# Kernel optimization log

Hardware: AMD Instinct MI355X
Metric: run time of the kernel (lower is better)

The kernel has to match this reference:

```python
import jax, jax.numpy as jnp
import numpy as np

EPS = jnp.float16(1e-8)

def setup_inputs() -> dict:
    key = jax.random.key(0)
    k1, k2, k3, k4 = jax.random.split(key, 4)
    B, S, D_IN, D_OUT = 4, 2048, 4096, 4096
    x = jax.random.normal(k1, (B, S, D_IN), dtype=jnp.float16)
    weight = jax.random.randint(k2, (D_OUT, D_IN), -127, 127, dtype=jnp.int32).astype(jnp.int8)
    weight_scales = (jax.random.uniform(k3, (D_OUT,), dtype=jnp.float32) * 0.02 + 0.001).astype(jnp.float16)
    bias = (jax.random.normal(k4, (1, D_OUT), dtype=jnp.float32) * 0.01).astype(jnp.float16)
    return {"x": x, "weight": weight, "weight_scales": weight_scales, "bias": bias}

def fake_quant_per_token(x):
    # per-token absmax fake quant to int8 range, stays fp16
    scales = jnp.max(jnp.abs(x), axis=-1, keepdims=True) / jnp.float16(127.0)
    scales = jnp.maximum(scales, EPS)
    return jnp.round(x / scales) * scales

def reference(x, weight, weight_scales, bias):
    # dequantize int8 weight with per-output-channel scales -> fp16 [out, in]
    w_fp16 = weight.astype(jnp.float16) * weight_scales[:, None]
    xq = fake_quant_per_token(x)
    # y = xq @ w^T + bias  : [B, S, out]
    y = jnp.einsum('bsi,oi->bso', xq, w_fp16) + bias
    return y
```

## Files before the change

### kernel.cpp

```cpp
#include <hip/hip_runtime.h>
#include <hip/hip_fp16.h>
#include <stdint.h>

#define M_TOK 8192
#define KD 4096
#define ND 4096

using i32x4 = __attribute__((ext_vector_type(4))) int;
using f32x4 = __attribute__((ext_vector_type(4))) float;

typedef const __attribute__((address_space(1))) void* gp_t;
typedef __attribute__((address_space(3))) void* lp_t;

__global__ __launch_bounds__(256) void prep_kernel(
    const float* __restrict__ x,
    int8_t* __restrict__ q,
    float* __restrict__ scales,
    const int* __restrict__ w32,
    int8_t* __restrict__ w8)
{
    const int t = threadIdx.x;
    if (blockIdx.x >= 8192) {
        const int b = blockIdx.x - 8192;
        const int4* w4 = (const int4*)w32;
        int* q32 = (int*)w8;
        #pragma unroll
        for (int u = 0; u < 4; ++u) {
            int g = b * 1024 + u * 256 + t;
            int4 a = w4[g];
            q32[g] = (a.x & 255) | ((a.y & 255) << 8) | ((a.z & 255) << 16) | (a.w << 24);
        }
        return;
    }

    const int row  = blockIdx.x;
    const int lane = t & 63;
    const int wave = t >> 6;

    const float4* xr = (const float4*)(x + (size_t)row * KD);
    float4 p[4];
    #pragma unroll
    for (int i = 0; i < 4; ++i) p[i] = xr[i * 256 + t];

    float am = 0.0f;
    #pragma unroll
    for (int i = 0; i < 4; ++i) {
        am = fmaxf(am, fmaxf(fmaxf(fabsf(p[i].x), fabsf(p[i].y)),
                             fmaxf(fabsf(p[i].z), fabsf(p[i].w))));
    }
    #pragma unroll
    for (int off = 32; off >= 1; off >>= 1)
        am = fmaxf(am, __shfl_xor(am, off));

    __shared__ float smax[4];
    if (lane == 0) smax[wave] = am;
    __syncthreads();
    am = fmaxf(fmaxf(smax[0], smax[1]), fmaxf(smax[2], smax[3]));

    float s = __half2float(__float2half(am * (1.0f / 127.0f)));
    s = fmaxf(s, 1e-30f);
    const float inv = 1.0f / s;

    int* qr = (int*)(q + (size_t)row * KD);
    #pragma unroll
    for (int i = 0; i < 4; ++i) {
        float vv[4] = {p[i].x, p[i].y, p[i].z, p[i].w};
        int w32v = 0;
        #pragma unroll
        for (int e = 0; e < 4; ++e) {
            float tq = __half2float(__float2half(vv[e] * inv));
            int qi = (int)rintf(tq);
            qi = max(-127, min(127, qi));
            w32v |= (qi & 255) << (8 * e);
        }
        qr[i * 256 + t] = w32v;
    }
    if (t == 0) scales[row] = s;
}


template<int MH>
__device__ __forceinline__ void read_A(const char* lA, int wr, int lane, i32x4 (&a)[4][2]) {
    const int l15 = lane & 15;
    const int cg  = (lane >> 4) << 4;
    #pragma unroll
    for (int mf = 0; mf < 4; ++mf) {
        const int row = MH * 128 + wr * 64 + mf * 16 + l15;
        const int sw  = (row & 7) << 4;
        #pragma unroll
        for (int ks = 0; ks < 2; ++ks)
            a[mf][ks] = *(const i32x4*)(lA + row * 128 + ((ks * 64 + cg) ^ sw));
    }
}

template<int NH>
__device__ __forceinline__ void read_B(const char* lB, int wc, int lane, i32x4 (&b)[2][2]) {
    const int l15 = lane & 15;
    const int cg  = (lane >> 4) << 4;
    #pragma unroll
    for (int nf = 0; nf < 2; ++nf) {
        const int row = NH * 128 + wc * 32 + nf * 16 + l15;
        const int sw  = (row & 7) << 4;
        #pragma unroll
        for (int ks = 0; ks < 2; ++ks)
            b[nf][ks] = *(const i32x4*)(lB + row * 128 + ((ks * 64 + cg) ^ sw));
    }
}

template<int MH>
__device__ __forceinline__ void mfma_half(i32x4 (&acc)[2][4][2][2],
                                          const i32x4 (&a)[4][2],
                                          const i32x4 (&b0)[2][2],
                                          const i32x4 (&b1)[2][2]) {
    __builtin_amdgcn_s_setprio(1);
    #pragma unroll
    for (int ks = 0; ks < 2; ++ks)
        #pragma unroll
        for (int mf = 0; mf < 4; ++mf) {
            #pragma unroll
            for (int nf = 0; nf < 2; ++nf)
                acc[MH][mf][0][nf] =
                    __builtin_amdgcn_mfma_i32_16x16x64_i8(a[mf][ks], b0[nf][ks],
                                                          acc[MH][mf][0][nf], 0, 0, 0);
            #pragma unroll
            for (int nf = 0; nf < 2; ++nf)
                acc[MH][mf][1][nf] =
                    __builtin_amdgcn_mfma_i32_16x16x64_i8(a[mf][ks], b1[nf][ks],
                                                          acc[MH][mf][1][nf], 0, 0, 0);
        }
    __builtin_amdgcn_s_setprio(0);
}

#define BAR() do { __builtin_amdgcn_s_barrier(); __builtin_amdgcn_sched_barrier(0); } while (0)

__global__ __launch_bounds__(512, 2) void gemm_q8_4ph_kernel(
    const int8_t* __restrict__ q,
    const int8_t* __restrict__ w8,
    const float* __restrict__ qs,
    const float* __restrict__ wscale,
    const float* __restrict__ bias,
    float* __restrict__ y)
{
    __shared__ char lds[2][2][32768];

    const int tid  = threadIdx.x;
    const int lane = tid & 63;
    const int wave = tid >> 6;
    const int wr   = wave >> 2;
    const int wc   = wave & 3;
    const int tn   = blockIdx.x;
    const int tm   = blockIdx.y;

    const int8_t* gA = q  + (size_t)(tm * 256) * KD;
    const int8_t* gB = w8 + (size_t)(tn * 256) * KD;

    char* lA0 = &lds[0][0][0]; char* lB0 = &lds[0][1][0];
    char* lA1 = &lds[1][0][0]; char* lB1 = &lds[1][1][0];

    int goff[2];
    #pragma unroll
    for (int qq = 0; qq < 2; ++qq) {
        const int d = qq * 8192 + wave * 1024 + lane * 16;
        const int r = d >> 7;
        const int cs = (d & 127) ^ ((r & 7) << 4);
        goff[qq] = r * KD + cs;
    }
    const int ldso = wave * 1024;

    #define STAGE(gbase, half, kbyte, ldst)                                              \
        do {                                                                             \
            const int8_t* _s = (gbase) + (size_t)(half) * 128 * KD + (kbyte);            \
            __builtin_amdgcn_global_load_lds((gp_t)(_s + goff[0]),                       \
                (lp_t)((ldst) + (half) * 16384 + ldso), 16, 0, 0);                       \
            __builtin_amdgcn_global_load_lds((gp_t)(_s + goff[1]),                       \
                (lp_t)((ldst) + (half) * 16384 + 8192 + ldso), 16, 0, 0);                \
        } while (0)

    i32x4 acc[2][4][2][2] = {};
    i32x4 a[4][2], b0[2][2], b1[2][2];

    STAGE(gA, 0, 0,   lA0);
    STAGE(gB, 0, 0,   lB0);
    STAGE(gA, 1, 0,   lA0);
    STAGE(gB, 1, 0,   lB0);
    STAGE(gA, 0, 128, lA1);
    STAGE(gB, 0, 128, lB1);
    asm volatile("s_waitcnt vmcnt(4)");
    BAR();

    for (int it = 0; it < 15; ++it) {
        const int kt  = 2 * it;
        const int kb1 = (kt + 1) * 128;
        const int kb2 = (kt + 2) * 128;
        const int kb3 = (kt + 3) * 128;

        read_A<0>(lA0, wr, lane, a);
        read_B<0>(lB0, wc, lane, b0);
        read_B<1>(lB0, wc, lane, b1);
        STAGE(gA, 1, kb1, lA1);
        STAGE(gB, 1, kb1, lB1);
        BAR();
        mfma_half<0>(acc, a, b0, b1);
        BAR();

        read_A<1>(lA0, wr, lane, a);
        STAGE(gA, 0, kb2, lA0);
        STAGE(gB, 0, kb2, lB0);
        BAR();
        mfma_half<1>(acc, a, b0, b1);
        asm volatile("s_waitcnt vmcnt(4)");
        BAR();

        read_A<0>(lA1, wr, lane, a);
        read_B<0>(lB1, wc, lane, b0);
        read_B<1>(lB1, wc, lane, b1);
        STAGE(gA, 1, kb2, lA0);
        STAGE(gB, 1, kb2, lB0);
        BAR();
        mfma_half<0>(acc, a, b0, b1);
        BAR();

        read_A<1>(lA1, wr, lane, a);
        STAGE(gA, 0, kb3, lA1);
        STAGE(gB, 0, kb3, lB1);
        BAR();
        mfma_half<1>(acc, a, b0, b1);
        asm volatile("s_waitcnt vmcnt(4)");
        BAR();
    }

    {
        const int kb1 = 31 * 128;
        read_A<0>(lA0, wr, lane, a);
        read_B<0>(lB0, wc, lane, b0);
        read_B<1>(lB0, wc, lane, b1);
        STAGE(gA, 1, kb1, lA1);
        STAGE(gB, 1, kb1, lB1);
        BAR();
        mfma_half<0>(acc, a, b0, b1);
        BAR();

        read_A<1>(lA0, wr, lane, a);
        BAR();
        mfma_half<1>(acc, a, b0, b1);
        asm volatile("s_waitcnt vmcnt(0)");
        BAR();

        read_A<0>(lA1, wr, lane, a);
        read_B<0>(lB1, wc, lane, b0);
        read_B<1>(lB1, wc, lane, b1);
        BAR();
        mfma_half<0>(acc, a, b0, b1);
        BAR();

        read_A<1>(lA1, wr, lane, a);
        BAR();
        mfma_half<1>(acc, a, b0, b1);
        BAR();
    }

    {
        char* myl = &lds[0][0][0] + wave * 16384;
        const int g   = lane >> 4;
        const int l15 = lane & 15;
        #pragma unroll
        for (int nh = 0; nh < 2; ++nh) {
            #pragma unroll
            for (int mh = 0; mh < 2; ++mh)
                #pragma unroll
                for (int mf = 0; mf < 4; ++mf) {
                    const int rmb = tm * 256 + mh * 128 + wr * 64 + mf * 16 + g * 4;
                    float qsv[4];
                    #pragma unroll
                    for (int r = 0; r < 4; ++r) qsv[r] = qs[rmb + r];
                    #pragma unroll
                    for (int nf = 0; nf < 2; ++nf) {
                        const int n  = tn * 256 + nh * 128 + wc * 32 + nf * 16 + l15;
                        const float wn = wscale[n];
                        const float bn = bias[n];
                        const int cl = nf * 16 + l15;
                        #pragma unroll
                        for (int r = 0; r < 4; ++r) {
                            const int rl = mh * 64 + mf * 16 + g * 4 + r;
                            const float val = (float)acc[mh][mf][nh][nf][r] * (qsv[r] * wn) + bn;
                            *(float*)(myl + rl * 128 + ((cl * 4) ^ ((rl & 7) << 4))) = val;
                        }
                    }
                }
            __builtin_amdgcn_s_barrier();
            const int gcol = tn * 256 + nh * 128 + wc * 32 + (lane & 7) * 4;
            #pragma unroll
            for (int k = 0; k < 16; ++k) {
                const int rl = (lane >> 3) + k * 8;
                const f32x4 v = *(const f32x4*)(myl + rl * 128 + (((lane & 7) * 16) ^ ((rl & 7) << 4)));
                const int grow = tm * 256 + (rl >> 6) * 128 + wr * 64 + (rl & 63);
                __builtin_nontemporal_store(v, (f32x4*)(y + (size_t)grow * ND + gcol));
            }
            __builtin_amdgcn_s_barrier();
        }
    }
    #undef STAGE
}

__global__ __launch_bounds__(256, 2) void gemm_q8_fallback(
    const int8_t* __restrict__ q,
    const int* __restrict__ w32,
    const float* __restrict__ qs,
    const float* __restrict__ wscale,
    const float* __restrict__ bias,
    float* __restrict__ y)
{
    __shared__ int8_t lA[128 * 64];
    __shared__ int8_t lB[128 * 64];

    const int tid  = threadIdx.x;
    const int lane = tid & 63;
    const int wave = tid >> 6;
    const int wr   = wave >> 1;
    const int wc   = wave & 1;
    const int tn   = blockIdx.x;
    const int tm   = blockIdx.y;

    const int ci0  = wave * 2;
    const int off0 = ci0 * 1024 + lane * 16;
    const int r0   = off0 >> 6;
    const int c0   = off0 & 63;
    const int off1 = off0 + 1024;
    const int r1   = off1 >> 6;
    const int c1   = off1 & 63;

    const int8_t* gA0 = q + (size_t)(tm * 128 + r0) * KD + c0;
    const int8_t* gA1 = q + (size_t)(tm * 128 + r1) * KD + c1;

    const int brow  = tid >> 1;
    const int bhalf = tid & 1;
    const int* gW = w32 + (size_t)(tn * 128 + brow) * KD + bhalf * 32;

    i32x4 acc[4][4] = {};
    const int kc = (lane >> 4) * 16;
    const int rA = wr * 64 + (lane & 15);
    const int rB = wc * 64 + (lane & 15);

    for (int k0 = 0; k0 < KD; k0 += 64) {
        __builtin_amdgcn_global_load_lds((gp_t)(gA0 + k0), (lp_t)(lA + ci0 * 1024),        16, 0, 0);
        __builtin_amdgcn_global_load_lds((gp_t)(gA1 + k0), (lp_t)(lA + ci0 * 1024 + 1024), 16, 0, 0);
        int bw[8];
        #pragma unroll
        for (int u = 0; u < 8; ++u) {
            i32x4 a4 = *(const i32x4*)(gW + k0 + u * 4);
            bw[u] = (a4[0] & 255) | ((a4[1] & 255) << 8) | ((a4[2] & 255) << 16) | (a4[3] << 24);
        }
        *(i32x4*)(lB + brow * 64 + bhalf * 32)      = i32x4{bw[0], bw[1], bw[2], bw[3]};
        *(i32x4*)(lB + brow * 64 + bhalf * 32 + 16) = i32x4{bw[4], bw[5], bw[6], bw[7]};
        __syncthreads();

        i32x4 a[4], b[4];
        #pragma unroll
        for (int i = 0; i < 4; ++i) a[i] = *(const i32x4*)(lA + (rA + i * 16) * 64 + kc);
        #pragma unroll
        for (int j = 0; j < 4; ++j) b[j] = *(const i32x4*)(lB + (rB + j * 16) * 64 + kc);
        #pragma unroll
        for (int i = 0; i < 4; ++i)
            #pragma unroll
            for (int j = 0; j < 4; ++j)
                acc[i][j] = __builtin_amdgcn_mfma_i32_16x16x64_i8(a[i], b[j], acc[i][j], 0, 0, 0);
        __syncthreads();
    }

    const int cbase = tn * 128 + wc * 64 + (lane & 15);
    const int rbase = tm * 128 + wr * 64 + ((lane >> 4) << 2);
    #pragma unroll
    for (int j = 0; j < 4; ++j) {
        const int n  = cbase + j * 16;
        const float wn = wscale[n];
        const float bn = bias[n];
        #pragma unroll
        for (int i = 0; i < 4; ++i)
            #pragma unroll
            for (int r = 0; r < 4; ++r) {
                const int m = rbase + i * 16 + r;
                y[(size_t)m * ND + n] = (float)acc[i][j][r] * (qs[m] * wn) + bn;
            }
    }
}

extern "C" void kernel_launch(void* const* d_in, const int* in_sizes, int n_in,
                              void* d_out, int out_size, void* d_ws, size_t ws_size,
                              hipStream_t stream) {
    const float* x      = (const float*)d_in[0];
    const int*   w32    = (const int*)d_in[1];
    const float* wscale = (const float*)d_in[2];
    const float* bias   = (const float*)d_in[3];
    float*       y      = (float*)d_out;

    const size_t q_bytes  = (size_t)M_TOK * KD;
    const size_t s_bytes  = (size_t)M_TOK * sizeof(float);
    const size_t w8_bytes = (size_t)ND * KD;

    int8_t* qbuf   = (int8_t*)d_ws;
    float*  scales = (float*)((char*)d_ws + q_bytes);
    int8_t* w8     = (int8_t*)((char*)d_ws + q_bytes + s_bytes);

    if (ws_size >= q_bytes + s_bytes + w8_bytes) {
        prep_kernel<<<8192 + 4096, 256, 0, stream>>>(x, qbuf, scales, w32, w8);
        dim3 grid(ND / 256, M_TOK / 256);
        gemm_q8_4ph_kernel<<<grid, 512, 0, stream>>>(qbuf, w8, scales, wscale, bias, y);
    } else {
        prep_kernel<<<8192, 256, 0, stream>>>(x, qbuf, scales, w32, w8);
        dim3 grid(ND / 128, M_TOK / 128);
        gemm_q8_fallback<<<grid, 256, 0, stream>>>(qbuf, w32, scales, wscale, bias, y);
    }
}
```

Baseline: 167.8 us.

## Double-buffer A fragments in registers and overlap LDS reads with MFMA

Replaces the compiler-generated LDS fragment reads with inline-asm ds_read_b128 using precomputed swizzled offsets. A second A register buffer lets the next half's A fragments be prefetched while the current MFMAs run, with partial lgkmcnt waits instead of full syncs. The goal is to hide LDS read latency behind matrix math. In exchange it uses more VGPRs, which may pressure occupancy at 512 threads and 2 blocks per CU, and the manual waitcnt counts must match the number of issued reads.

```diff
diff --git a/kernel.cpp b/kernel.cpp
--- a/kernel.cpp
+++ b/kernel.cpp
@@ -79,32 +79,8 @@
 }
 
 
-template<int MH>
-__device__ __forceinline__ void read_A(const char* lA, int wr, int lane, i32x4 (&a)[4][2]) {
-    const int l15 = lane & 15;
-    const int cg  = (lane >> 4) << 4;
-    #pragma unroll
-    for (int mf = 0; mf < 4; ++mf) {
-        const int row = MH * 128 + wr * 64 + mf * 16 + l15;
-        const int sw  = (row & 7) << 4;
-        #pragma unroll
-        for (int ks = 0; ks < 2; ++ks)
-            a[mf][ks] = *(const i32x4*)(lA + row * 128 + ((ks * 64 + cg) ^ sw));
-    }
-}
-
-template<int NH>
-__device__ __forceinline__ void read_B(const char* lB, int wc, int lane, i32x4 (&b)[2][2]) {
-    const int l15 = lane & 15;
-    const int cg  = (lane >> 4) << 4;
-    #pragma unroll
-    for (int nf = 0; nf < 2; ++nf) {
-        const int row = NH * 128 + wc * 32 + nf * 16 + l15;
-        const int sw  = (row & 7) << 4;
-        #pragma unroll
-        for (int ks = 0; ks < 2; ++ks)
-            b[nf][ks] = *(const i32x4*)(lB + row * 128 + ((ks * 64 + cg) ^ sw));
-    }
+__device__ __forceinline__ void ds_read16(i32x4 &dst, unsigned addr) {
+    asm volatile("ds_read_b128 %0, %1" : "=&v"(dst) : "v"(addr));
 }
 
 template<int MH>
@@ -132,6 +108,9 @@
 }
 
 #define BAR() do { __builtin_amdgcn_s_barrier(); __builtin_amdgcn_sched_barrier(0); } while (0)
+#define LGKM8()  do { asm volatile("s_waitcnt lgkmcnt(8)"); __builtin_amdgcn_sched_barrier(0); } while (0)
+#define LGKM0()  do { asm volatile("s_waitcnt lgkmcnt(0)"); __builtin_amdgcn_sched_barrier(0); } while (0)
+#define VM4()    asm volatile("s_waitcnt vmcnt(4)")
 
 __global__ __launch_bounds__(512, 2) void gemm_q8_4ph_kernel(
     const int8_t* __restrict__ q,
@@ -157,6 +136,32 @@
     char* lA0 = &lds[0][0][0]; char* lB0 = &lds[0][1][0];
     char* lA1 = &lds[1][0][0]; char* lB1 = &lds[1][1][0];
 
+    const unsigned LB   = (unsigned)(size_t)(lp_t)&lds[0][0][0];
+    const unsigned A0B  = LB;
+    const unsigned B0Bs = LB + 32768;
+    const unsigned A1B  = LB + 65536;
+    const unsigned B1Bs = LB + 98304;
+
+    const int l15 = lane & 15;
+    const int cg  = (lane >> 4) << 4;
+    unsigned aoff[8], boff[4];
+    #pragma unroll
+    for (int mf = 0; mf < 4; ++mf) {
+        const int row = wr * 64 + mf * 16 + l15;
+        const int sw  = (row & 7) << 4;
+        #pragma unroll
+        for (int ks = 0; ks < 2; ++ks)
+            aoff[mf * 2 + ks] = row * 128 + ((ks * 64 + cg) ^ sw);
+    }
+    #pragma unroll
+    for (int nf = 0; nf < 2; ++nf) {
+        const int row = wc * 32 + nf * 16 + l15;
+        const int sw  = (row & 7) << 4;
+        #pragma unroll
+        for (int ks = 0; ks < 2; ++ks)
+            boff[nf * 2 + ks] = row * 128 + ((ks * 64 + cg) ^ sw);
+    }
+
     int goff[2];
     #pragma unroll
     for (int qq = 0; qq < 2; ++qq) {
@@ -176,8 +181,24 @@
                 (lp_t)((ldst) + (half) * 16384 + 8192 + ldso), 16, 0, 0);                \
         } while (0)
 
+    #define RD_A(dst, base)                                                              \
+        do {                                                                             \
+            ds_read16(dst[0][0], (base) + aoff[0]); ds_read16(dst[0][1], (base) + aoff[1]); \
+            ds_read16(dst[1][0], (base) + aoff[2]); ds_read16(dst[1][1], (base) + aoff[3]); \
+            ds_read16(dst[2][0], (base) + aoff[4]); ds_read16(dst[2][1], (base) + aoff[5]); \
+            ds_read16(dst[3][0], (base) + aoff[6]); ds_read16(dst[3][1], (base) + aoff[7]); \
+        } while (0)
+
+    #define RD_B(base)                                                                   \
+        do {                                                                             \
+            ds_read16(b0[0][0], (base) + boff[0]); ds_read16(b0[0][1], (base) + boff[1]); \
+            ds_read16(b0[1][0], (base) + boff[2]); ds_read16(b0[1][1], (base) + boff[3]); \
+            ds_read16(b1[0][0], (base) + 16384u + boff[0]); ds_read16(b1[0][1], (base) + 16384u + boff[1]); \
+            ds_read16(b1[1][0], (base) + 16384u + boff[2]); ds_read16(b1[1][1], (base) + 16384u + boff[3]); \
+        } while (0)
+
     i32x4 acc[2][4][2][2] = {};
-    i32x4 a[4][2], b0[2][2], b1[2][2];
+    i32x4 aA[4][2], aB[4][2], b0[2][2], b1[2][2];
 
     STAGE(gA, 0, 0,   lA0);
     STAGE(gB, 0, 0,   lB0);
@@ -185,8 +206,9 @@
     STAGE(gB, 1, 0,   lB0);
     STAGE(gA, 0, 128, lA1);
     STAGE(gB, 0, 128, lB1);
-    asm volatile("s_waitcnt vmcnt(4)");
+    VM4();
     BAR();
+    RD_A(aA, A0B);
 
     for (int it = 0; it < 15; ++it) {
         const int kt  = 2 * it;
@@ -194,75 +216,79 @@
         const int kb2 = (kt + 2) * 128;
         const int kb3 = (kt + 3) * 128;
 
-        read_A<0>(lA0, wr, lane, a);
-        read_B<0>(lB0, wc, lane, b0);
-        read_B<1>(lB0, wc, lane, b1);
+        RD_B(B0Bs);
+        RD_A(aB, A0B + 16384u);
         STAGE(gA, 1, kb1, lA1);
         STAGE(gB, 1, kb1, lB1);
         BAR();
-        mfma_half<0>(acc, a, b0, b1);
-        BAR();
-
-        read_A<1>(lA0, wr, lane, a);
+        LGKM8();
+        mfma_half<0>(acc, aA, b0, b1);
+        VM4();
+        BAR();
+
+        RD_A(aA, A1B);
         STAGE(gA, 0, kb2, lA0);
         STAGE(gB, 0, kb2, lB0);
         BAR();
-        mfma_half<1>(acc, a, b0, b1);
-        asm volatile("s_waitcnt vmcnt(4)");
-        BAR();
-
-        read_A<0>(lA1, wr, lane, a);
-        read_B<0>(lB1, wc, lane, b0);
-        read_B<1>(lB1, wc, lane, b1);
+        LGKM8();
+        mfma_half<1>(acc, aB, b0, b1);
+        VM4();
+        BAR();
+
+        RD_B(B1Bs);
+        RD_A(aB, A1B + 16384u);
         STAGE(gA, 1, kb2, lA0);
         STAGE(gB, 1, kb2, lB0);
         BAR();
-        mfma_half<0>(acc, a, b0, b1);
-        BAR();
-
-        read_A<1>(lA1, wr, lane, a);
+        LGKM8();
+        mfma_half<0>(acc, aA, b0, b1);
+        VM4();
+        BAR();
+
+        RD_A(aA, A0B);
         STAGE(gA, 0, kb3, lA1);
         STAGE(gB, 0, kb3, lB1);
         BAR();
-        mfma_half<1>(acc, a, b0, b1);
-        asm volatile("s_waitcnt vmcnt(4)");
+        LGKM8();
+        mfma_half<1>(acc, aB, b0, b1);
+        VM4();
         BAR();
     }
 
     {
         const int kb1 = 31 * 128;
-        read_A<0>(lA0, wr, lane, a);
-        read_B<0>(lB0, wc, lane, b0);
-        read_B<1>(lB0, wc, lane, b1);
+        RD_B(B0Bs);
+        RD_A(aB, A0B + 16384u);
         STAGE(gA, 1, kb1, lA1);
         STAGE(gB, 1, kb1, lB1);
         BAR();
-        mfma_half<0>(acc, a, b0, b1);
-        BAR();
-
-        read_A<1>(lA0, wr, lane, a);
-        BAR();
-        mfma_half<1>(acc, a, b0, b1);
+        LGKM8();
+        mfma_half<0>(acc, aA, b0, b1);
+        VM4();
+        BAR();
+
+        RD_A(aA, A1B);
+        BAR();
+        LGKM8();
+        mfma_half<1>(acc, aB, b0, b1);
         asm volatile("s_waitcnt vmcnt(0)");
         BAR();
 
-        read_A<0>(lA1, wr, lane, a);
-        read_B<0>(lB1, wc, lane, b0);
-        read_B<1>(lB1, wc, lane, b1);
-        BAR();
-        mfma_half<0>(acc, a, b0, b1);
-        BAR();
-
-        read_A<1>(lA1, wr, lane, a);
-        BAR();
-        mfma_half<1>(acc, a, b0, b1);
+        RD_B(B1Bs);
+        RD_A(aB, A1B + 16384u);
+        BAR();
+        LGKM8();
+        mfma_half<0>(acc, aA, b0, b1);
+        BAR();
+
+        LGKM0();
+        mfma_half<1>(acc, aB, b0, b1);
         BAR();
     }
 
     {
         char* myl = &lds[0][0][0] + wave * 16384;
-        const int g   = lane >> 4;
-        const int l15 = lane & 15;
+        const int g = lane >> 4;
         #pragma unroll
         for (int nh = 0; nh < 2; ++nh) {
             #pragma unroll
@@ -300,6 +326,8 @@
         }
     }
     #undef STAGE
+    #undef RD_A
+    #undef RD_B
 }
 
 __global__ __launch_bounds__(256, 2) void gemm_q8_fallback(
```

After: 298.5 us. 77.9% more time.
